# Optimization experiments

Measured on AMD Instinct MI355X. Metric: run time of the kernel, lower is better.

The kernel has to match this reference:

```python
import jax, jax.numpy as jnp
import numpy as np

L = 8       # num decoder layers
S = 192     # seq_len = h*w = 24*8
D = 512     # d_model
DFF = 2048  # dim_feedforward
H, W, BS = 24, 8, 16
EPS = 1e-5


def setup_inputs() -> dict:
    key = jax.random.key(0)
    ks = jax.random.split(key, 8)
    f = jax.random.normal
    return {
        "q_feat": f(ks[0], (BS, D * L, H, W), jnp.float32),
        "g_feat": f(ks[1], (BS, D * L, H, W), jnp.float32),
        "targets": jax.random.randint(ks[2], (BS,), 0, 8),
        "score_embed": f(ks[3], (L, S, S), jnp.float32) * 0.05,
        "fc0_w": f(ks[4], (L, D, D), jnp.float32) * (1.0 / np.sqrt(D)),
        "fc0_b": jnp.zeros((L, D), jnp.float32),
        "bn1_g": jnp.ones((L,), jnp.float32),
        "bn1_b": jnp.zeros((L,), jnp.float32),
        "fc2_w": f(ks[5], (L, DFF, S), jnp.float32) * (1.0 / np.sqrt(S)),
        "fc2_b": jnp.zeros((L, DFF), jnp.float32),
        "bn2_g": jnp.ones((L, DFF), jnp.float32),
        "bn2_b": jnp.zeros((L, DFF), jnp.float32),
        "fc3_w": f(ks[6], (L, DFF), jnp.float32) * (1.0 / np.sqrt(DFF)),
        "fc3_b": jnp.zeros((L,), jnp.float32),
        "bn3_g": jnp.ones((L,), jnp.float32),
        "bn3_b": jnp.zeros((L,), jnp.float32),
    }


def _layer(qf, gf, se, w0, b0, g1, b1, w2, b2, g2, bb2, w3, b3, g3, bb3):
    # qf: [q,s,d], gf: [k,s,d]; shared fc0 projection for query and key
    query = jnp.einsum('qsd,ed->qse', qf, w0) + b0
    key_ = jnp.einsum('ksd,ed->kse', gf, w0) + b0
    # 4D correlation volume masked by sigmoid of learned score embedding
    score = jnp.einsum('qtd,ksd->qkst', query, key_) * jax.nn.sigmoid(se)
    q, k = score.shape[0], score.shape[1]
    sc = score.reshape(q * k, S, S)
    cat = jnp.concatenate([sc.max(axis=1), sc.max(axis=2)], axis=-1)  # [qk, 2S]
    x = cat.reshape(-1, S)  # [2qk, S]  (matches torch view(-1,1,S))
    # bn1: single channel -> normalize over all elements (training-mode BN)
    x = g1 * (x - x.mean()) * jax.lax.rsqrt(x.var() + EPS) + b1
    x = x @ w2.T + b2  # [2qk, DFF]
    mu = x.mean(0)
    var = x.var(0)
    x = g2 * (x - mu) * jax.lax.rsqrt(var + EPS) + bb2
    x = jax.nn.relu(x)
    x = x @ w3 + b3  # [2qk]
    x = x.reshape(-1, 2).sum(-1)  # [qk]: sum of row-max branch and col-max branch
    x = g3 * (x - x.mean()) * jax.lax.rsqrt(x.var() + EPS) + bb3
    return x.reshape(q, k)


def reference(q_feat, g_feat, targets, score_embed, fc0_w, fc0_b, bn1_g, bn1_b,
              fc2_w, fc2_b, bn2_g, bn2_b, fc3_w, fc3_b, bn3_g, bn3_b):
    bs = q_feat.shape[0]
    qf = jnp.transpose(q_feat, (0, 2, 3, 1)).reshape(bs, S, D * L)
    gf = jnp.transpose(g_feat, (0, 2, 3, 1)).reshape(bs, S, D * L)
    score = None
    for i in range(L):  # fixed small layer loop; each layer has distinct params
        si = _layer(qf[..., i * D:(i + 1) * D], gf[..., i * D:(i + 1) * D],
                    score_embed[i], fc0_w[i], fc0_b[i], bn1_g[i], bn1_b[i],
                    fc2_w[i], fc2_b[i], bn2_g[i], bn2_b[i],
                    fc3_w[i], fc3_b[i], bn3_g[i], bn3_b[i])
        score = si if score is None else score + si
    pair_labels = (targets[:, None] == targets[None, :]).astype(jnp.float32)
    return score, pair_labels
```

## Files before the change

kernel.cpp:

```cpp
#include <hip/hip_runtime.h>
#include <hip/hip_bf16.h>


#define EPS_ 1e-5f

typedef __attribute__((ext_vector_type(8))) _Float16 fp16x8;
typedef __attribute__((ext_vector_type(4)))  float   f32x4;
typedef __attribute__((ext_vector_type(16))) float   f32x16;

__device__ __forceinline__ unsigned fkey(float f) {
    unsigned u = __float_as_uint(f);
    return (u & 0x80000000u) ? ~u : (u | 0x80000000u);
}
__device__ __forceinline__ float funkey(unsigned k) {
    return (k & 0x80000000u) ? __uint_as_float(k & 0x7FFFFFFFu)
                             : __uint_as_float(~k);
}
__device__ __forceinline__ void gld16(const void* gp, void* lp) {
    __builtin_amdgcn_global_load_lds(
        (const __attribute__((address_space(1))) unsigned*)gp,
        (__attribute__((address_space(3))) unsigned*)lp, 16, 0, 0);
}

__global__ __launch_bounds__(256) void k_sig(const float* __restrict__ se,
                                             float* __restrict__ sig) {
    int i = blockIdx.x * 256 + threadIdx.x;
    float4 v = *(const float4*)(se + (size_t)i * 4);
    float4 o;
    o.x = 1.f / (1.f + __expf(-v.x));
    o.y = 1.f / (1.f + __expf(-v.y));
    o.z = 1.f / (1.f + __expf(-v.z));
    o.w = 1.f / (1.f + __expf(-v.w));
    *(float4*)(sig + (size_t)i * 4) = o;
}

__global__ __launch_bounds__(256) void k_fc0(const float* __restrict__ qfeat,
                                             const float* __restrict__ gfeat,
                                             const float* __restrict__ w0,
                                             const float* __restrict__ b0,
                                             _Float16* __restrict__ Qh) {
    int bid = blockIdx.x;
    int et = bid & 1;  bid >>= 1;
    int tt = bid % 3;  bid /= 3;
    int b  = bid & 15; bid >>= 4;
    int l  = bid & 7;  bid >>= 3;
    int sel = bid;
    const float* feat  = sel ? gfeat : qfeat;
    const float* Af = feat + (size_t)b * 4096 * 192 + (size_t)l * 512 * 192;
    const float* Wf = w0 + (size_t)l * 262144;
    int t0 = tt * 64, e0 = et * 256;

    __shared__ __align__(16) char At[64 * 80];
    __shared__ __align__(16) char Bt[256 * 80];

    int tid = threadIdx.x;
    int lane = tid & 63;
    int w = tid >> 6;
    int half = lane >> 5;
    int lrow = lane & 31;

    f32x16 acc[2][2];
    #pragma unroll
    for (int mi = 0; mi < 2; mi++)
        #pragma unroll
        for (int ni = 0; ni < 2; ni++)
            #pragma unroll
            for (int r = 0; r < 16; r++) acc[mi][ni][r] = 0.f;

    for (int d0 = 0; d0 < 512; d0 += 32) {
        __syncthreads();
        {
            int tA = tid & 63;
            int dp = tid >> 6;
            #pragma unroll
            for (int r = 0; r < 4; r++) {
                int d = dp * 2 + r * 8;
                float v0 = Af[(size_t)(d0 + d) * 192 + t0 + tA];
                float v1 = Af[(size_t)(d0 + d + 1) * 192 + t0 + tA];
                _Float16 h2[2] = {(_Float16)v0, (_Float16)v1};
                *(unsigned*)(At + tA * 80 + d * 2) = *(unsigned*)h2;
            }
        }
        {
            #pragma unroll
            for (int p = 0; p < 8; p++) {
                int s = tid + p * 256;
                int e = s >> 3;
                int q = s & 7;
                float4 wv = *(const float4*)(Wf + (size_t)(e0 + e) * 512 + d0 + q * 4);
                _Float16 h[4] = {(_Float16)wv.x, (_Float16)wv.y, (_Float16)wv.z, (_Float16)wv.w};
                *(uint2*)(Bt + e * 80 + q * 8) = *(uint2*)h;
            }
        }
        __syncthreads();
        #pragma unroll
        for (int ks = 0; ks < 2; ks++) {
            int koff = ks * 32 + half * 16;
            fp16x8 a[2], bf[2];
            #pragma unroll
            for (int mi = 0; mi < 2; mi++)
                a[mi] = *(const fp16x8*)(At + (mi * 32 + lrow) * 80 + koff);
            #pragma unroll
            for (int ni = 0; ni < 2; ni++)
                bf[ni] = *(const fp16x8*)(Bt + (w * 64 + ni * 32 + lrow) * 80 + koff);
            #pragma unroll
            for (int mi = 0; mi < 2; mi++)
                #pragma unroll
                for (int ni = 0; ni < 2; ni++)
                    acc[mi][ni] = __builtin_amdgcn_mfma_f32_32x32x16_f16(a[mi], bf[ni], acc[mi][ni], 0, 0, 0);
        }
    }

    _Float16* Obase = Qh + ((size_t)(sel * 8 + l) * 16 + b) * 98304;
    #pragma unroll
    for (int ni = 0; ni < 2; ni++) {
        int e = e0 + w * 64 + ni * 32 + lrow;
        float bias = b0[l * 512 + e];
        #pragma unroll
        for (int mi = 0; mi < 2; mi++) {
            #pragma unroll
            for (int r = 0; r < 16; r++) {
                int t = t0 + mi * 32 + (r & 3) + 8 * (r >> 2) + 4 * half;
                Obase[(size_t)t * 512 + e] = (_Float16)(acc[mi][ni][r] + bias);
            }
        }
    }
}

__global__ __launch_bounds__(256) void k_cvt(const float* __restrict__ src,
                                             _Float16* __restrict__ dst) {
    int i = blockIdx.x * 256 + threadIdx.x;
    float4 v = *(const float4*)(src + (size_t)i * 4);
    _Float16 h[4] = {(_Float16)v.x, (_Float16)v.y, (_Float16)v.z, (_Float16)v.w};
    *(uint2*)(dst + (size_t)i * 4) = *(uint2*)h;
}

__global__ __launch_bounds__(256) void k_score(const _Float16* __restrict__ Qh,
                                               const float* __restrict__ sig,
                                               unsigned* __restrict__ xkey) {
    int bid = blockIdx.x;
    int l = bid / 576;
    int rem = bid - l * 576;
    int grp = rem / 96;
    int within = rem - grp * 96;
    int mt = within >> 2;
    int nt = grp * 4 + (within & 3);
    int m0 = mt * 128, n0 = nt * 128;

    const char* Ag = (const char*)(Qh + (size_t)(8 + l) * 1572864);
    const char* Bg = (const char*)(Qh + (size_t)l * 1572864);
    const float* sg = sig + (size_t)l * 36864;

    __shared__ __align__(16) char As[8192];
    __shared__ __align__(16) char Bs[8192];
    __shared__ unsigned tmaxL[4][64];
    __shared__ unsigned smaxL[4][64];

    int tid = threadIdx.x;
    int lane = tid & 63;
    int w = tid >> 6;
    int wm = w >> 1, wn = w & 1;

    f32x4 acc[4][4];
    #pragma unroll
    for (int mi = 0; mi < 4; mi++)
        #pragma unroll
        for (int nj = 0; nj < 4; nj++)
            #pragma unroll
            for (int r = 0; r < 4; r++) acc[mi][nj][r] = 0.f;

    int srow = lane >> 2;
    int sseg = ((lane & 3) ^ ((srow >> 1) & 3)) * 16;
    int c = lane & 15;
    int kqp = (((lane >> 4) ^ ((c >> 1) & 3))) * 16;

    for (int d0 = 0; d0 < 1024; d0 += 64) {
        __syncthreads();
        #pragma unroll
        for (int j = 0; j < 2; j++) {
            int r = w * 32 + j * 16 + srow;
            gld16(Ag + (size_t)(m0 + r) * 1024 + d0 + sseg, As + (w * 32 + j * 16) * 64);
            gld16(Bg + (size_t)(n0 + r) * 1024 + d0 + sseg, Bs + (w * 32 + j * 16) * 64);
        }
        __syncthreads();
        fp16x8 a[4], b[4];
        #pragma unroll
        for (int mi = 0; mi < 4; mi++)
            a[mi] = *(const fp16x8*)(As + (wm * 64 + mi * 16 + c) * 64 + kqp);
        #pragma unroll
        for (int nj = 0; nj < 4; nj++)
            b[nj] = *(const fp16x8*)(Bs + (wn * 64 + nj * 16 + c) * 64 + kqp);
        #pragma unroll
        for (int mi = 0; mi < 4; mi++)
            #pragma unroll
            for (int nj = 0; nj < 4; nj++)
                acc[mi][nj] = __builtin_amdgcn_mfma_f32_16x16x32_f16(a[mi], b[nj], acc[mi][nj], 0, 0, 0);
    }

    int gmb = m0 + wm * 64;
    int kk = gmb / 192, sb = gmb - kk * 192;
    int gnb = n0 + wn * 64;
    int qq = gnb / 192, tb = gnb - qq * 192;
    int rq = (lane >> 4) * 4;

    float rowm[4][4];
    float colm[4];
    #pragma unroll
    for (int mi = 0; mi < 4; mi++)
        #pragma unroll
        for (int r = 0; r < 4; r++) rowm[mi][r] = -3.4e38f;
    #pragma unroll
    for (int nj = 0; nj < 4; nj++) colm[nj] = -3.4e38f;

    #pragma unroll
    for (int mi = 0; mi < 4; mi++) {
        #pragma unroll
        for (int r = 0; r < 4; r++) {
            int s = sb + mi * 16 + rq + r;
            const float* srow_p = sg + (size_t)s * 192 + tb;
            #pragma unroll
            for (int nj = 0; nj < 4; nj++) {
                float m = srow_p[nj * 16 + c];
                float v = acc[mi][nj][r] * m;
                rowm[mi][r] = fmaxf(rowm[mi][r], v);
                colm[nj] = fmaxf(colm[nj], v);
            }
        }
    }
    #pragma unroll
    for (int nj = 0; nj < 4; nj++) {
        colm[nj] = fmaxf(colm[nj], __shfl_xor(colm[nj], 16));
        colm[nj] = fmaxf(colm[nj], __shfl_xor(colm[nj], 32));
    }
    if (lane < 16) {
        #pragma unroll
        for (int nj = 0; nj < 4; nj++)
            tmaxL[wm * 2 + wn][nj * 16 + lane] = fkey(colm[nj]);
    }
    #pragma unroll
    for (int st = 1; st <= 8; st <<= 1)
        #pragma unroll
        for (int mi = 0; mi < 4; mi++)
            #pragma unroll
            for (int r = 0; r < 4; r++)
                rowm[mi][r] = fmaxf(rowm[mi][r], __shfl_xor(rowm[mi][r], st));
    if (c == 0) {
        #pragma unroll
        for (int mi = 0; mi < 4; mi++)
            #pragma unroll
            for (int r = 0; r < 4; r++)
                smaxL[wm * 2 + wn][mi * 16 + rq + r] = fkey(rowm[mi][r]);
    }
    __syncthreads();

    #pragma unroll
    for (int rep = 0; rep < 2; rep++) {
        int idx = tid + rep * 256;
        int wp = idx >> 7;
        int which = (idx >> 6) & 1;
        int off = idx & 63;
        int wmf = wp >> 1, wnf = wp & 1;
        int kf = (m0 + wmf * 64) / 192, sbf = (m0 + wmf * 64) % 192;
        int qf = (n0 + wnf * 64) / 192, tbf = (n0 + wnf * 64) % 192;
        int jp = qf * 16 + kf;
        if (which == 0)
            atomicMax(&xkey[((size_t)l * 512 + 2 * jp) * 192 + tbf + off], tmaxL[wp][off]);
        else
            atomicMax(&xkey[((size_t)l * 512 + 2 * jp + 1) * 192 + sbf + off], smaxL[wp][off]);
    }
}

__global__ __launch_bounds__(256) void k_bn1s(const unsigned* __restrict__ xkey,
                                              float* __restrict__ bn1acc) {
    int l = blockIdx.x / 48;
    int b = blockIdx.x - l * 48;
    const unsigned* xk = xkey + (size_t)l * 98304 + b * 2048;
    int tid = threadIdx.x;
    uint4 v1 = *(const uint4*)(xk + tid * 8);
    uint4 v2 = *(const uint4*)(xk + tid * 8 + 4);
    float s = 0.f, s2 = 0.f;
    float e;
    e = funkey(v1.x); s += e; s2 += e * e;
    e = funkey(v1.y); s += e; s2 += e * e;
    e = funkey(v1.z); s += e; s2 += e * e;
    e = funkey(v1.w); s += e; s2 += e * e;
    e = funkey(v2.x); s += e; s2 += e * e;
    e = funkey(v2.y); s += e; s2 += e * e;
    e = funkey(v2.z); s += e; s2 += e * e;
    e = funkey(v2.w); s += e; s2 += e * e;
    #pragma unroll
    for (int o = 32; o; o >>= 1) { s += __shfl_down(s, o); s2 += __shfl_down(s2, o); }
    if ((tid & 63) == 0) {
        atomicAdd(&bn1acc[l * 2], s);
        atomicAdd(&bn1acc[l * 2 + 1], s2);
    }
}

__global__ __launch_bounds__(256) void k_bn1n(const unsigned* __restrict__ xkey,
                                              const float* __restrict__ bn1acc,
                                              const float* __restrict__ g1,
                                              const float* __restrict__ b1,
                                              _Float16* __restrict__ xh) {
    int idx = blockIdx.x * 256 + threadIdx.x;
    int l = idx / 24576;
    float mu = bn1acc[l * 2] * (1.f / 98304.f);
    float var = bn1acc[l * 2 + 1] * (1.f / 98304.f) - mu * mu;
    float a1 = g1[l] * rsqrtf(var + EPS_);
    float c1 = b1[l] - mu * a1;
    uint4 kv = *(const uint4*)(xkey + (size_t)idx * 4);
    _Float16 h[4];
    h[0] = (_Float16)(funkey(kv.x) * a1 + c1);
    h[1] = (_Float16)(funkey(kv.y) * a1 + c1);
    h[2] = (_Float16)(funkey(kv.z) * a1 + c1);
    h[3] = (_Float16)(funkey(kv.w) * a1 + c1);
    *(uint2*)(xh + (size_t)idx * 4) = *(uint2*)h;
}

__global__ __launch_bounds__(256) void k_fc2(const _Float16* __restrict__ xh,
                                             const _Float16* __restrict__ w2h,
                                             const float* __restrict__ b2,
                                             _Float16* __restrict__ hb,
                                             float* __restrict__ bn2sum,
                                             float* __restrict__ bn2sq) {
    int bid = blockIdx.x;
    int l = bid >> 6;
    int rem = bid & 63;
    int mt = rem & 3, nt = rem >> 2;
    int m0 = mt * 128, n0 = nt * 128;
    const char* Ag = (const char*)(xh + (size_t)l * 98304);
    const char* Bg = (const char*)(w2h + (size_t)l * 393216);

    __shared__ __align__(16) char As[8192];
    __shared__ __align__(16) char Bs[8192];

    int tid = threadIdx.x;
    int lane = tid & 63;
    int w = tid >> 6;
    int wm = w >> 1, wn = w & 1;

    f32x4 acc[4][4];
    #pragma unroll
    for (int mi = 0; mi < 4; mi++)
        #pragma unroll
        for (int nj = 0; nj < 4; nj++)
            #pragma unroll
            for (int r = 0; r < 4; r++) acc[mi][nj][r] = 0.f;

    int srow = lane >> 2;
    int sseg = ((lane & 3) ^ ((srow >> 1) & 3)) * 16;
    int c = lane & 15;
    int kqp = (((lane >> 4) ^ ((c >> 1) & 3))) * 16;

    for (int d0 = 0; d0 < 384; d0 += 64) {
        __syncthreads();
        #pragma unroll
        for (int j = 0; j < 2; j++) {
            int r = w * 32 + j * 16 + srow;
            gld16(Ag + (size_t)(m0 + r) * 384 + d0 + sseg, As + (w * 32 + j * 16) * 64);
            gld16(Bg + (size_t)(n0 + r) * 384 + d0 + sseg, Bs + (w * 32 + j * 16) * 64);
        }
        __syncthreads();
        fp16x8 a[4], b[4];
        #pragma unroll
        for (int mi = 0; mi < 4; mi++)
            a[mi] = *(const fp16x8*)(As + (wm * 64 + mi * 16 + c) * 64 + kqp);
        #pragma unroll
        for (int nj = 0; nj < 4; nj++)
            b[nj] = *(const fp16x8*)(Bs + (wn * 64 + nj * 16 + c) * 64 + kqp);
        #pragma unroll
        for (int mi = 0; mi < 4; mi++)
            #pragma unroll
            for (int nj = 0; nj < 4; nj++)
                acc[mi][nj] = __builtin_amdgcn_mfma_f32_16x16x32_f16(a[mi], b[nj], acc[mi][nj], 0, 0, 0);
    }

    int rq = (lane >> 4) * 4;
    _Float16* ho = hb + (size_t)l * 1048576;
    float colsum[4], colsq[4];
    #pragma unroll
    for (int nj = 0; nj < 4; nj++) { colsum[nj] = 0.f; colsq[nj] = 0.f; }
    #pragma unroll
    for (int nj = 0; nj < 4; nj++) {
        int gf = n0 + wn * 64 + nj * 16 + c;
        float bias = b2[l * 2048 + gf];
        #pragma unroll
        for (int mi = 0; mi < 4; mi++) {
            #pragma unroll
            for (int r = 0; r < 4; r++) {
                int gm = m0 + wm * 64 + mi * 16 + rq + r;
                float v = acc[mi][nj][r] + bias;
                ho[(size_t)gm * 2048 + gf] = (_Float16)v;
                colsum[nj] += v;
                colsq[nj] += v * v;
            }
        }
    }
    #pragma unroll
    for (int nj = 0; nj < 4; nj++) {
        colsum[nj] += __shfl_xor(colsum[nj], 16);
        colsum[nj] += __shfl_xor(colsum[nj], 32);
        colsq[nj]  += __shfl_xor(colsq[nj], 16);
        colsq[nj]  += __shfl_xor(colsq[nj], 32);
    }
    if (lane < 16) {
        #pragma unroll
        for (int nj = 0; nj < 4; nj++) {
            int gf = n0 + wn * 64 + nj * 16 + lane;
            atomicAdd(&bn2sum[l * 2048 + gf], colsum[nj]);
            atomicAdd(&bn2sq[l * 2048 + gf], colsq[nj]);
        }
    }
}

__global__ __launch_bounds__(256) void k_fc3(const _Float16* __restrict__ hb,
                                             const float* __restrict__ bn2sum,
                                             const float* __restrict__ bn2sq,
                                             const float* __restrict__ g2,
                                             const float* __restrict__ bb2,
                                             const float* __restrict__ w3,
                                             const float* __restrict__ b3,
                                             float* __restrict__ ybuf) {
    int n = blockIdx.x & 511;
    int l = blockIdx.x >> 9;
    const _Float16* h = hb + ((size_t)l * 512 + n) * 2048;
    int tid = threadIdx.x;
    int f0 = tid * 8;
    fp16x8 hv = *(const fp16x8*)(h + f0);
    float sum = 0.f;
    #pragma unroll
    for (int j = 0; j < 8; j++) {
        int f = f0 + j;
        float mu = bn2sum[l * 2048 + f] * (1.f / 512.f);
        float var = bn2sq[l * 2048 + f] * (1.f / 512.f) - mu * mu;
        float a2 = g2[l * 2048 + f] * rsqrtf(var + EPS_);
        float c2 = bb2[l * 2048 + f] - mu * a2;
        float v = (float)hv[j] * a2 + c2;
        v = fmaxf(v, 0.f);
        sum += v * w3[l * 2048 + f];
    }
    __shared__ float red[4];
    int lane = tid & 63, w = tid >> 6;
    #pragma unroll
    for (int o = 32; o; o >>= 1) sum += __shfl_down(sum, o);
    if (lane == 0) red[w] = sum;
    __syncthreads();
    if (tid == 0) ybuf[l * 512 + n] = red[0] + red[1] + red[2] + red[3] + b3[l];
}

__global__ __launch_bounds__(256) void k_final(const float* __restrict__ ybuf,
                                               const float* __restrict__ g3,
                                               const float* __restrict__ bb3,
                                               const int* __restrict__ targets,
                                               float* __restrict__ out) {
    int tid = threadIdx.x;
    __shared__ float red[8];
    float scoreacc = 0.f;
    for (int l = 0; l < 8; l++) {
        float z = ybuf[l * 512 + 2 * tid] + ybuf[l * 512 + 2 * tid + 1];
        float s = z, s2 = z * z;
        int lane = tid & 63, w = tid >> 6;
        #pragma unroll
        for (int o = 32; o; o >>= 1) { s += __shfl_down(s, o); s2 += __shfl_down(s2, o); }
        if (lane == 0) { red[w] = s; red[4 + w] = s2; }
        __syncthreads();
        float S1 = red[0] + red[1] + red[2] + red[3];
        float S2 = red[4] + red[5] + red[6] + red[7];
        float mu = S1 * (1.f / 256.f);
        float var = S2 * (1.f / 256.f) - mu * mu;
        float rstd = rsqrtf(var + EPS_);
        scoreacc += g3[l] * (z - mu) * rstd + bb3[l];
        __syncthreads();
    }
    out[tid] = scoreacc;
    int i = tid >> 4, j = tid & 15;
    out[256 + tid] = (targets[i] == targets[j]) ? 1.f : 0.f;
}

extern "C" void kernel_launch(void* const* d_in, const int* in_sizes, int n_in,
                              void* d_out, int out_size, void* d_ws, size_t ws_size,
                              hipStream_t stream) {
    const float* q_feat = (const float*)d_in[0];
    const float* g_feat = (const float*)d_in[1];
    const int*   targets = (const int*)d_in[2];
    const float* se     = (const float*)d_in[3];
    const float* fc0_w  = (const float*)d_in[4];
    const float* fc0_b  = (const float*)d_in[5];
    const float* bn1_g  = (const float*)d_in[6];
    const float* bn1_b  = (const float*)d_in[7];
    const float* fc2_w  = (const float*)d_in[8];
    const float* fc2_b  = (const float*)d_in[9];
    const float* bn2_g  = (const float*)d_in[10];
    const float* bn2_b  = (const float*)d_in[11];
    const float* fc3_w  = (const float*)d_in[12];
    const float* fc3_b  = (const float*)d_in[13];
    const float* bn3_g  = (const float*)d_in[14];
    const float* bn3_b  = (const float*)d_in[15];

    float* ws = (float*)d_ws;
    _Float16* Qh   = (_Float16*)ws;
    float*    sig  = ws + 12582912;
    unsigned* xkey = (unsigned*)(ws + 12877824);
    _Float16* xh   = (_Float16*)(ws + 13664256);
    _Float16* w2h  = (_Float16*)(ws + 14057472);
    _Float16* hb   = (_Float16*)(ws + 15630336);
    float* bn2sum = ws + 19824640;
    float* bn2sq  = ws + 19841024;
    float* bn1acc = ws + 19857408;
    float* ybuf   = ws + 19857424;
    float* out  = (float*)d_out;

    hipMemsetAsync(xkey, 0, 786432 * sizeof(unsigned), stream);
    hipMemsetAsync(bn2sum, 0, (2 * 16384 + 16) * sizeof(float), stream);
    k_sig<<<288, 256, 0, stream>>>(se, sig);
    k_cvt<<<3072, 256, 0, stream>>>(fc2_w, w2h);
    k_fc0<<<1536, 256, 0, stream>>>(q_feat, g_feat, fc0_w, fc0_b, Qh);
    k_score<<<4608, 256, 0, stream>>>(Qh, sig, xkey);
    k_bn1s<<<384, 256, 0, stream>>>(xkey, bn1acc);
    k_bn1n<<<768, 256, 0, stream>>>(xkey, bn1acc, bn1_g, bn1_b, xh);
    k_fc2<<<512, 256, 0, stream>>>(xh, w2h, fc2_b, hb, bn2sum, bn2sq);
    k_fc3<<<4096, 256, 0, stream>>>(hb, bn2sum, bn2sq, bn2_g, bn2_b, fc3_w, fc3_b, ybuf);
    k_final<<<1, 256, 0, stream>>>(ybuf, bn3_g, bn3_b, targets, out);
}
```

Before: 432.9 us.

## Rewrite score GEMM as 256x256 tiles with double-buffered LDS pipeline

Restructures the correlation-volume GEMM kernel from 128x128 tiles with 256 threads to 256x256 tiles with 512 threads. It uses 128KB of double-buffered LDS with async global-to-LDS loads interleaved between MFMA phases, and raises wave priority around the matrix math. The block order is also interleaved across layers. The larger tiles are meant to raise arithmetic intensity and hide load latency, at the cost of heavy register and LDS use, which limits occupancy.

```diff
diff --git a/kernel.cpp b/kernel.cpp
--- a/kernel.cpp
+++ b/kernel.cpp
@@ -135,138 +135,212 @@
     *(uint2*)(dst + (size_t)i * 4) = *(uint2*)h;
 }
 
-__global__ __launch_bounds__(256) void k_score(const _Float16* __restrict__ Qh,
-                                               const float* __restrict__ sig,
-                                               unsigned* __restrict__ xkey) {
+#define FENCE asm volatile("" ::: "memory")
+#define BAR() do { FENCE; __builtin_amdgcn_s_barrier(); FENCE; } while (0)
+
+__global__ __launch_bounds__(512, 2) void k_score(const _Float16* __restrict__ Qh,
+                                                  const float* __restrict__ sig,
+                                                  unsigned* __restrict__ xkey) {
     int bid = blockIdx.x;
-    int l = bid / 576;
-    int rem = bid - l * 576;
-    int grp = rem / 96;
-    int within = rem - grp * 96;
-    int mt = within >> 2;
-    int nt = grp * 4 + (within & 3);
-    int m0 = mt * 128, n0 = nt * 128;
+    int l = bid & 7;
+    int tau = bid >> 3;
+    int mt = tau % 12;
+    int nt = tau / 12;
+    int m0 = mt * 256, n0 = nt * 256;
 
     const char* Ag = (const char*)(Qh + (size_t)(8 + l) * 1572864);
     const char* Bg = (const char*)(Qh + (size_t)l * 1572864);
-    const float* sg = sig + (size_t)l * 36864;
-
-    __shared__ __align__(16) char As[8192];
-    __shared__ __align__(16) char Bs[8192];
-    __shared__ unsigned tmaxL[4][64];
-    __shared__ unsigned smaxL[4][64];
+
+    __shared__ __align__(16) char smem[131072];
 
     int tid = threadIdx.x;
     int lane = tid & 63;
     int w = tid >> 6;
-    int wm = w >> 1, wn = w & 1;
-
-    f32x4 acc[4][4];
-    #pragma unroll
-    for (int mi = 0; mi < 4; mi++)
+    int wm = w >> 2, wn = w & 3;
+    int c = lane & 15;
+    int hi4 = lane >> 4;
+
+    int pk0 = ((hi4)     ^ (c & 7)) * 16;
+    int pk1 = ((4 + hi4) ^ (c & 7)) * 16;
+    char* aBase = smem + wm * 16384 + c * 128;
+    char* bBase = smem + 65536 + (wn >> 1) * 16384 + ((wn & 1) * 64 + c) * 128;
+
+    int rl = lane >> 3;
+    int qsw = ((lane & 7) ^ rl) * 16;
+    const char* Asrc = Ag + (size_t)(m0 + w * 8 + rl) * 1024 + qsw;
+    const char* Bsrc = Bg + (size_t)(n0 + w * 8 + rl) * 1024 + qsw;
+    char* aSt = smem + w * 1024;
+    char* bSt = smem + 65536 + w * 1024;
+
+    f32x4 acc[8][4];
+    #pragma unroll
+    for (int mi = 0; mi < 8; mi++)
         #pragma unroll
         for (int nj = 0; nj < 4; nj++)
             #pragma unroll
             for (int r = 0; r < 4; r++) acc[mi][nj][r] = 0.f;
 
-    int srow = lane >> 2;
-    int sseg = ((lane & 3) ^ ((srow >> 1) & 3)) * 16;
-    int c = lane & 15;
-    int kqp = (((lane >> 4) ^ ((c >> 1) & 3))) * 16;
-
-    for (int d0 = 0; d0 < 1024; d0 += 64) {
-        __syncthreads();
-        #pragma unroll
-        for (int j = 0; j < 2; j++) {
-            int r = w * 32 + j * 16 + srow;
-            gld16(Ag + (size_t)(m0 + r) * 1024 + d0 + sseg, As + (w * 32 + j * 16) * 64);
-            gld16(Bg + (size_t)(n0 + r) * 1024 + d0 + sseg, Bs + (w * 32 + j * 16) * 64);
-        }
-        __syncthreads();
-        fp16x8 a[4], b[4];
-        #pragma unroll
-        for (int mi = 0; mi < 4; mi++)
-            a[mi] = *(const fp16x8*)(As + (wm * 64 + mi * 16 + c) * 64 + kqp);
-        #pragma unroll
-        for (int nj = 0; nj < 4; nj++)
-            b[nj] = *(const fp16x8*)(Bs + (wn * 64 + nj * 16 + c) * 64 + kqp);
-        #pragma unroll
-        for (int mi = 0; mi < 4; mi++)
-            #pragma unroll
-            for (int nj = 0; nj < 4; nj++)
-                acc[mi][nj] = __builtin_amdgcn_mfma_f32_16x16x32_f16(a[mi], b[nj], acc[mi][nj], 0, 0, 0);
-    }
-
-    int gmb = m0 + wm * 64;
-    int kk = gmb / 192, sb = gmb - kk * 192;
-    int gnb = n0 + wn * 64;
-    int qq = gnb / 192, tb = gnb - qq * 192;
-    int rq = (lane >> 4) * 4;
-
-    float rowm[4][4];
-    float colm[4];
-    #pragma unroll
-    for (int mi = 0; mi < 4; mi++)
+    fp16x8 a[4][2], b01[2][2], b23[2][2];
+
+    auto STA = [&](int t, int h) {
+        if (t < 8) {
+            const char* s = Asrc + (size_t)(h * 128) * 1024 + t * 128;
+            char* d = aSt + (t & 1) * 32768 + h * 16384;
+            gld16(s, d);
+            gld16(s + 64 * 1024, d + 8192);
+        }
+    };
+    auto STB = [&](int t, int h) {
+        if (t < 8) {
+            const char* s = Bsrc + (size_t)(h * 128) * 1024 + t * 128;
+            char* d = bSt + (t & 1) * 32768 + h * 16384;
+            gld16(s, d);
+            gld16(s + 64 * 1024, d + 8192);
+        }
+    };
+    auto LDA = [&](int t, int mh) {
+        const char* p = aBase + (t & 1) * 32768 + mh * 8192;
+        #pragma unroll
+        for (int m = 0; m < 4; m++) {
+            a[m][0] = *(const fp16x8*)(p + m * 2048 + pk0);
+            a[m][1] = *(const fp16x8*)(p + m * 2048 + pk1);
+        }
+    };
+    auto LDB = [&](int t, int nh, fp16x8 (&bb)[2][2]) {
+        const char* p = bBase + (t & 1) * 32768 + nh * 4096;
+        #pragma unroll
+        for (int n = 0; n < 2; n++) {
+            bb[n][0] = *(const fp16x8*)(p + n * 2048 + pk0);
+            bb[n][1] = *(const fp16x8*)(p + n * 2048 + pk1);
+        }
+    };
+    auto MM = [&](int mh, int nh, fp16x8 (&bb)[2][2]) {
+        #pragma unroll
+        for (int ks = 0; ks < 2; ks++)
+            #pragma unroll
+            for (int m = 0; m < 4; m++)
+                #pragma unroll
+                for (int n = 0; n < 2; n++)
+                    acc[mh * 4 + m][nh * 2 + n] = __builtin_amdgcn_mfma_f32_16x16x32_f16(
+                        a[m][ks], bb[n][ks], acc[mh * 4 + m][nh * 2 + n], 0, 0, 0);
+    };
+
+    STB(0, 0); STB(0, 1); STA(0, 0); STA(0, 1); STB(1, 0); STB(1, 1);
+    asm volatile("s_waitcnt vmcnt(4)" ::: "memory");
+    BAR();
+
+    #pragma unroll
+    for (int it = 0; it < 4; it++) {
+        int T = 2 * it, U = 2 * it + 1;
+        LDA(T, 0); LDB(T, 0, b01); STA(U, 0); BAR();
+        __builtin_amdgcn_s_setprio(1); MM(0, 0, b01); __builtin_amdgcn_s_setprio(0); BAR();
+        LDB(T, 1, b23); STA(U, 1); BAR();
+        __builtin_amdgcn_s_setprio(1); MM(0, 1, b23); __builtin_amdgcn_s_setprio(0); BAR();
+        LDA(T, 1); STB(T + 2, 0); BAR();
+        __builtin_amdgcn_s_setprio(1); MM(1, 0, b01); __builtin_amdgcn_s_setprio(0); BAR();
+        STB(T + 2, 1); BAR();
+        __builtin_amdgcn_s_setprio(1); MM(1, 1, b23); __builtin_amdgcn_s_setprio(0);
+        if (it < 3) { asm volatile("s_waitcnt vmcnt(4)" ::: "memory"); }
+        else        { asm volatile("s_waitcnt vmcnt(0)" ::: "memory"); }
+        BAR();
+        LDA(U, 0); LDB(U, 0, b01); STA(T + 2, 0); BAR();
+        __builtin_amdgcn_s_setprio(1); MM(0, 0, b01); __builtin_amdgcn_s_setprio(0); BAR();
+        LDB(U, 1, b23); STA(T + 2, 1); BAR();
+        __builtin_amdgcn_s_setprio(1); MM(0, 1, b23); __builtin_amdgcn_s_setprio(0); BAR();
+        LDA(U, 1); STB(T + 3, 0); BAR();
+        __builtin_amdgcn_s_setprio(1); MM(1, 0, b01); __builtin_amdgcn_s_setprio(0); BAR();
+        STB(T + 3, 1); BAR();
+        __builtin_amdgcn_s_setprio(1); MM(1, 1, b23); __builtin_amdgcn_s_setprio(0);
+        if (it < 3) { asm volatile("s_waitcnt vmcnt(4)" ::: "memory"); }
+        BAR();
+    }
+
+    int rq = hi4 * 4;
+    int gcb = n0 + wn * 64;
+    int qq = gcb / 192;
+    int tb = gcb - qq * 192;
+    (void)qq;
+    const float* sg = sig + (size_t)l * 36864;
+
+    float rowm[8][4];
+    float colm[2][4];
+    #pragma unroll
+    for (int mi = 0; mi < 8; mi++)
         #pragma unroll
         for (int r = 0; r < 4; r++) rowm[mi][r] = -3.4e38f;
     #pragma unroll
-    for (int nj = 0; nj < 4; nj++) colm[nj] = -3.4e38f;
-
-    #pragma unroll
-    for (int mi = 0; mi < 4; mi++) {
+    for (int h = 0; h < 2; h++)
+        #pragma unroll
+        for (int nj = 0; nj < 4; nj++) colm[h][nj] = -3.4e38f;
+
+    #pragma unroll
+    for (int mi = 0; mi < 8; mi++) {
+        int gm = m0 + wm * 128 + mi * 16;
+        int sb = gm % 192;
         #pragma unroll
         for (int r = 0; r < 4; r++) {
-            int s = sb + mi * 16 + rq + r;
-            const float* srow_p = sg + (size_t)s * 192 + tb;
+            const float* sp = sg + (size_t)(sb + rq + r) * 192 + tb;
             #pragma unroll
             for (int nj = 0; nj < 4; nj++) {
-                float m = srow_p[nj * 16 + c];
-                float v = acc[mi][nj][r] * m;
+                float v = acc[mi][nj][r] * sp[nj * 16 + c];
                 rowm[mi][r] = fmaxf(rowm[mi][r], v);
-                colm[nj] = fmaxf(colm[nj], v);
+                colm[mi >> 2][nj] = fmaxf(colm[mi >> 2][nj], v);
             }
         }
     }
     #pragma unroll
-    for (int nj = 0; nj < 4; nj++) {
-        colm[nj] = fmaxf(colm[nj], __shfl_xor(colm[nj], 16));
-        colm[nj] = fmaxf(colm[nj], __shfl_xor(colm[nj], 32));
-    }
-    if (lane < 16) {
-        #pragma unroll
-        for (int nj = 0; nj < 4; nj++)
-            tmaxL[wm * 2 + wn][nj * 16 + lane] = fkey(colm[nj]);
-    }
-    #pragma unroll
     for (int st = 1; st <= 8; st <<= 1)
         #pragma unroll
-        for (int mi = 0; mi < 4; mi++)
+        for (int mi = 0; mi < 8; mi++)
             #pragma unroll
             for (int r = 0; r < 4; r++)
                 rowm[mi][r] = fmaxf(rowm[mi][r], __shfl_xor(rowm[mi][r], st));
+    #pragma unroll
+    for (int h = 0; h < 2; h++)
+        #pragma unroll
+        for (int nj = 0; nj < 4; nj++) {
+            colm[h][nj] = fmaxf(colm[h][nj], __shfl_xor(colm[h][nj], 16));
+            colm[h][nj] = fmaxf(colm[h][nj], __shfl_xor(colm[h][nj], 32));
+        }
+
+    unsigned* red = (unsigned*)smem;
     if (c == 0) {
         #pragma unroll
-        for (int mi = 0; mi < 4; mi++)
+        for (int mi = 0; mi < 8; mi++)
             #pragma unroll
             for (int r = 0; r < 4; r++)
-                smaxL[wm * 2 + wn][mi * 16 + rq + r] = fkey(rowm[mi][r]);
+                red[w * 256 + mi * 16 + rq + r] = fkey(rowm[mi][r]);
+    }
+    if (lane < 16) {
+        #pragma unroll
+        for (int h = 0; h < 2; h++)
+            #pragma unroll
+            for (int nj = 0; nj < 4; nj++)
+                red[w * 256 + 128 + h * 64 + nj * 16 + lane] = fkey(colm[h][nj]);
     }
     __syncthreads();
-
-    #pragma unroll
-    for (int rep = 0; rep < 2; rep++) {
-        int idx = tid + rep * 256;
-        int wp = idx >> 7;
-        int which = (idx >> 6) & 1;
-        int off = idx & 63;
-        int wmf = wp >> 1, wnf = wp & 1;
-        int kf = (m0 + wmf * 64) / 192, sbf = (m0 + wmf * 64) % 192;
-        int qf = (n0 + wnf * 64) / 192, tbf = (n0 + wnf * 64) % 192;
-        int jp = qf * 16 + kf;
-        if (which == 0)
-            atomicMax(&xkey[((size_t)l * 512 + 2 * jp) * 192 + tbf + off], tmaxL[wp][off]);
-        else
-            atomicMax(&xkey[((size_t)l * 512 + 2 * jp + 1) * 192 + sbf + off], smaxL[wp][off]);
+    #pragma unroll
+    for (int pass = 0; pass < 4; pass++) {
+        int flat = pass * 512 + tid;
+        unsigned val = red[flat];
+        int ww = flat >> 8;
+        int rem = flat & 255;
+        int wmf = ww >> 2, wnf = ww & 3;
+        int gcbf = n0 + wnf * 64;
+        int qqf = gcbf / 192;
+        size_t addr;
+        if (rem < 128) {
+            int gmf = m0 + wmf * 128 + rem;
+            int kkf = gmf / 192;
+            int sf = gmf - kkf * 192;
+            addr = ((size_t)l * 512 + 2 * (qqf * 16 + kkf) + 1) * 192 + sf;
+        } else {
+            int ii = rem - 128;
+            int hh = ii >> 6, cc = ii & 63;
+            int kkf = (m0 + wmf * 128 + hh * 64) / 192;
+            addr = ((size_t)l * 512 + 2 * (qqf * 16 + kkf)) * 192 + (gcbf - qqf * 192) + cc;
+        }
+        atomicMax(&xkey[addr], val);
     }
 }
 
@@ -514,7 +588,7 @@
     k_sig<<<288, 256, 0, stream>>>(se, sig);
     k_cvt<<<3072, 256, 0, stream>>>(fc2_w, w2h);
     k_fc0<<<1536, 256, 0, stream>>>(q_feat, g_feat, fc0_w, fc0_b, Qh);
-    k_score<<<4608, 256, 0, stream>>>(Qh, sig, xkey);
+    k_score<<<1152, 512, 0, stream>>>(Qh, sig, xkey);
     k_bn1s<<<384, 256, 0, stream>>>(xkey, bn1acc);
     k_bn1n<<<768, 256, 0, stream>>>(xkey, bn1acc, bn1_g, bn1_b, xh);
     k_fc2<<<512, 256, 0, stream>>>(xh, w2h, fc2_b, hb, bn2sum, bn2sq);
```

Result: faster. 412.7 us (-4.7%).

## Pipeline score GEMM with triple-buffered LDS and fuse prep kernels

Applied to the files above, without the earlier changes.

Rewrites the correlation-score kernel as 512-thread blocks with 256x128 tiles and a three-slot LDS ring, so global-to-LDS loads for later K steps run while the current MFMAs execute. It uses explicit vmcnt waits, raw barriers and setprio. The sigmoid, weight conversion and two memsets are merged into one prep kernel to cut launch overhead. Block ordering changes so that layer index varies fastest. The large shared footprint may limit occupancy, and the hand-written waitcnt sequence is fragile.

```diff
diff --git a/kernel.cpp b/kernel.cpp
--- a/kernel.cpp
+++ b/kernel.cpp
@@ -22,16 +22,40 @@
         (__attribute__((address_space(3))) unsigned*)lp, 16, 0, 0);
 }
 
-__global__ __launch_bounds__(256) void k_sig(const float* __restrict__ se,
-                                             float* __restrict__ sig) {
-    int i = blockIdx.x * 256 + threadIdx.x;
-    float4 v = *(const float4*)(se + (size_t)i * 4);
-    float4 o;
-    o.x = 1.f / (1.f + __expf(-v.x));
-    o.y = 1.f / (1.f + __expf(-v.y));
-    o.z = 1.f / (1.f + __expf(-v.z));
-    o.w = 1.f / (1.f + __expf(-v.w));
-    *(float4*)(sig + (size_t)i * 4) = o;
+__global__ __launch_bounds__(256) void k_prep(const float* __restrict__ se,
+                                              float* __restrict__ sig,
+                                              const float* __restrict__ w2,
+                                              _Float16* __restrict__ w2h,
+                                              unsigned* __restrict__ xkey,
+                                              float* __restrict__ bn2z) {
+    int b = blockIdx.x;
+    int tid = threadIdx.x;
+    if (b < 3072) {
+        int i = b * 256 + tid;
+        float4 v = *(const float4*)(w2 + (size_t)i * 4);
+        _Float16 h[4] = {(_Float16)v.x, (_Float16)v.y, (_Float16)v.z, (_Float16)v.w};
+        *(uint2*)(w2h + (size_t)i * 4) = *(uint2*)h;
+    } else if (b < 3360) {
+        int i = (b - 3072) * 256 + tid;
+        float4 v = *(const float4*)(se + (size_t)i * 4);
+        float4 o;
+        o.x = 1.f / (1.f + __expf(-v.x));
+        o.y = 1.f / (1.f + __expf(-v.y));
+        o.z = 1.f / (1.f + __expf(-v.z));
+        o.w = 1.f / (1.f + __expf(-v.w));
+        *(float4*)(sig + (size_t)i * 4) = o;
+    } else if (b < 3552) {
+        int i = (b - 3360) * 256 + tid;
+        uint4 z = {0u, 0u, 0u, 0u};
+        uint4* p = (uint4*)xkey + (size_t)i * 4;
+        p[0] = z; p[1] = z; p[2] = z; p[3] = z;
+    } else {
+        int i = (b - 3552) * 256 + tid;
+        if (i < 8196) {
+            float4 z = {0.f, 0.f, 0.f, 0.f};
+            *(float4*)(bn2z + (size_t)i * 4) = z;
+        }
+    }
 }
 
 __global__ __launch_bounds__(256) void k_fc0(const float* __restrict__ qfeat,
@@ -127,39 +151,39 @@
     }
 }
 
-__global__ __launch_bounds__(256) void k_cvt(const float* __restrict__ src,
-                                             _Float16* __restrict__ dst) {
-    int i = blockIdx.x * 256 + threadIdx.x;
-    float4 v = *(const float4*)(src + (size_t)i * 4);
-    _Float16 h[4] = {(_Float16)v.x, (_Float16)v.y, (_Float16)v.z, (_Float16)v.w};
-    *(uint2*)(dst + (size_t)i * 4) = *(uint2*)h;
-}
-
-__global__ __launch_bounds__(256) void k_score(const _Float16* __restrict__ Qh,
-                                               const float* __restrict__ sig,
-                                               unsigned* __restrict__ xkey) {
+#define BARP() do { __builtin_amdgcn_s_barrier(); \
+                    __builtin_amdgcn_sched_barrier(0); } while (0)
+
+__global__ __launch_bounds__(512, 4) void k_score(const _Float16* __restrict__ Qh,
+                                                  const float* __restrict__ sig,
+                                                  unsigned* __restrict__ xkey) {
     int bid = blockIdx.x;
-    int l = bid / 576;
-    int rem = bid - l * 576;
-    int grp = rem / 96;
-    int within = rem - grp * 96;
-    int mt = within >> 2;
-    int nt = grp * 4 + (within & 3);
-    int m0 = mt * 128, n0 = nt * 128;
+    int l = bid & 7;
+    int tau = bid >> 3;
+    int mt = tau % 12;
+    int nt = tau / 12;
+    int m0 = mt * 256, n0 = nt * 128;
 
     const char* Ag = (const char*)(Qh + (size_t)(8 + l) * 1572864);
     const char* Bg = (const char*)(Qh + (size_t)l * 1572864);
-    const float* sg = sig + (size_t)l * 36864;
-
-    __shared__ __align__(16) char As[8192];
-    __shared__ __align__(16) char Bs[8192];
-    __shared__ unsigned tmaxL[4][64];
-    __shared__ unsigned smaxL[4][64];
+
+    __shared__ __align__(16) char smem[73728];
+    __shared__ unsigned tmaxL[8][64];
+    __shared__ unsigned smaxL[8][64];
 
     int tid = threadIdx.x;
     int lane = tid & 63;
     int w = tid >> 6;
     int wm = w >> 1, wn = w & 1;
+    int c = lane & 15;
+    int hi4 = lane >> 4;
+
+    int pk = (hi4 ^ (c & 3)) * 16;
+
+    int r4 = lane >> 2;
+    int qsw = ((lane & 3) ^ (r4 & 3)) * 16;
+    const char* AsrcL = Ag + (size_t)(m0 + w * 16 + r4) * 1024 + qsw;
+    const char* BsrcL = Bg + (size_t)(n0 + w * 16 + r4) * 1024 + qsw;
 
     f32x4 acc[4][4];
     #pragma unroll
@@ -169,39 +193,61 @@
             #pragma unroll
             for (int r = 0; r < 4; r++) acc[mi][nj][r] = 0.f;
 
-    int srow = lane >> 2;
-    int sseg = ((lane & 3) ^ ((srow >> 1) & 3)) * 16;
-    int c = lane & 15;
-    int kqp = (((lane >> 4) ^ ((c >> 1) & 3))) * 16;
-
-    for (int d0 = 0; d0 < 1024; d0 += 64) {
-        __syncthreads();
-        #pragma unroll
-        for (int j = 0; j < 2; j++) {
-            int r = w * 32 + j * 16 + srow;
-            gld16(Ag + (size_t)(m0 + r) * 1024 + d0 + sseg, As + (w * 32 + j * 16) * 64);
-            gld16(Bg + (size_t)(n0 + r) * 1024 + d0 + sseg, Bs + (w * 32 + j * 16) * 64);
-        }
-        __syncthreads();
-        fp16x8 a[4], b[4];
+    fp16x8 a[4], b[4];
+
+    auto STAGE = [&](int t) {
+        if (t < 16) {
+            int slot = t % 3;
+            const char* sa = AsrcL + t * 64;
+            char* da = smem + slot * 16384 + w * 1024;
+            gld16(sa, da);
+            gld16(sa + 131072, da + 8192);
+            gld16(BsrcL + t * 64, smem + 49152 + slot * 8192 + w * 1024);
+        }
+    };
+    auto LDAB = [&](int t) {
+        int slot = t % 3;
+        const char* pa = smem + slot * 16384 + (wm * 64 + c) * 64;
         #pragma unroll
         for (int mi = 0; mi < 4; mi++)
-            a[mi] = *(const fp16x8*)(As + (wm * 64 + mi * 16 + c) * 64 + kqp);
+            a[mi] = *(const fp16x8*)(pa + mi * 1024 + pk);
+        const char* pb = smem + 49152 + slot * 8192 + (wn * 64 + c) * 64;
         #pragma unroll
         for (int nj = 0; nj < 4; nj++)
-            b[nj] = *(const fp16x8*)(Bs + (wn * 64 + nj * 16 + c) * 64 + kqp);
+            b[nj] = *(const fp16x8*)(pb + nj * 1024 + pk);
+    };
+
+    STAGE(0); STAGE(1);
+    asm volatile("s_waitcnt vmcnt(3)");
+    BARP();
+
+    #pragma unroll
+    for (int t = 0; t < 16; t++) {
+        LDAB(t);
+        STAGE(t + 2);
+        BARP();
+        __builtin_amdgcn_s_setprio(1);
         #pragma unroll
         for (int mi = 0; mi < 4; mi++)
             #pragma unroll
             for (int nj = 0; nj < 4; nj++)
                 acc[mi][nj] = __builtin_amdgcn_mfma_f32_16x16x32_f16(a[mi], b[nj], acc[mi][nj], 0, 0, 0);
-    }
-
+        __builtin_amdgcn_s_setprio(0);
+        if (t < 14)       { asm volatile("s_waitcnt vmcnt(3)"); }
+        else if (t == 14) { asm volatile("s_waitcnt vmcnt(0)"); }
+        BARP();
+    }
+
+    __syncthreads();
+
+    int rq = hi4 * 4;
     int gmb = m0 + wm * 64;
     int kk = gmb / 192, sb = gmb - kk * 192;
+    (void)kk;
     int gnb = n0 + wn * 64;
     int qq = gnb / 192, tb = gnb - qq * 192;
-    int rq = (lane >> 4) * 4;
+    (void)qq;
+    const float* sg = sig + (size_t)l * 36864;
 
     float rowm[4][4];
     float colm[4];
@@ -217,11 +263,10 @@
         #pragma unroll
         for (int r = 0; r < 4; r++) {
             int s = sb + mi * 16 + rq + r;
-            const float* srow_p = sg + (size_t)s * 192 + tb;
+            const float* sp = sg + (size_t)s * 192 + tb;
             #pragma unroll
             for (int nj = 0; nj < 4; nj++) {
-                float m = srow_p[nj * 16 + c];
-                float v = acc[mi][nj][r] * m;
+                float v = acc[mi][nj][r] * sp[nj * 16 + c];
                 rowm[mi][r] = fmaxf(rowm[mi][r], v);
                 colm[nj] = fmaxf(colm[nj], v);
             }
@@ -235,7 +280,7 @@
     if (lane < 16) {
         #pragma unroll
         for (int nj = 0; nj < 4; nj++)
-            tmaxL[wm * 2 + wn][nj * 16 + lane] = fkey(colm[nj]);
+            tmaxL[w][nj * 16 + lane] = fkey(colm[nj]);
     }
     #pragma unroll
     for (int st = 1; st <= 8; st <<= 1)
@@ -249,24 +294,27 @@
         for (int mi = 0; mi < 4; mi++)
             #pragma unroll
             for (int r = 0; r < 4; r++)
-                smaxL[wm * 2 + wn][mi * 16 + rq + r] = fkey(rowm[mi][r]);
+                smaxL[w][mi * 16 + rq + r] = fkey(rowm[mi][r]);
     }
     __syncthreads();
 
     #pragma unroll
-    for (int rep = 0; rep < 2; rep++) {
-        int idx = tid + rep * 256;
-        int wp = idx >> 7;
+    for (int pass = 0; pass < 2; pass++) {
+        int idx = pass * 512 + tid;
+        int ww = idx >> 7;
         int which = (idx >> 6) & 1;
         int off = idx & 63;
-        int wmf = wp >> 1, wnf = wp & 1;
-        int kf = (m0 + wmf * 64) / 192, sbf = (m0 + wmf * 64) % 192;
-        int qf = (n0 + wnf * 64) / 192, tbf = (n0 + wnf * 64) % 192;
-        int jp = qf * 16 + kf;
-        if (which == 0)
-            atomicMax(&xkey[((size_t)l * 512 + 2 * jp) * 192 + tbf + off], tmaxL[wp][off]);
-        else
-            atomicMax(&xkey[((size_t)l * 512 + 2 * jp + 1) * 192 + sbf + off], smaxL[wp][off]);
+        int wmf = ww >> 1, wnf = ww & 1;
+        int gmf = m0 + wmf * 64;
+        int kkf = gmf / 192, sbf = gmf - kkf * 192;
+        int gnf = n0 + wnf * 64;
+        int qqf = gnf / 192, tbf = gnf - qqf * 192;
+        int jp = qqf * 16 + kkf;
+        size_t addr;
+        unsigned val;
+        if (which == 0) { val = tmaxL[ww][off]; addr = ((size_t)l * 512 + 2 * jp) * 192 + tbf + off; }
+        else            { val = smaxL[ww][off]; addr = ((size_t)l * 512 + 2 * jp + 1) * 192 + sbf + off; }
+        atomicMax(&xkey[addr], val);
     }
 }
 
@@ -509,12 +557,9 @@
     float* ybuf   = ws + 19857424;
     float* out  = (float*)d_out;
 
-    hipMemsetAsync(xkey, 0, 786432 * sizeof(unsigned), stream);
-    hipMemsetAsync(bn2sum, 0, (2 * 16384 + 16) * sizeof(float), stream);
-    k_sig<<<288, 256, 0, stream>>>(se, sig);
-    k_cvt<<<3072, 256, 0, stream>>>(fc2_w, w2h);
+    k_prep<<<3585, 256, 0, stream>>>(se, sig, fc2_w, w2h, xkey, bn2sum);
     k_fc0<<<1536, 256, 0, stream>>>(q_feat, g_feat, fc0_w, fc0_b, Qh);
-    k_score<<<4608, 256, 0, stream>>>(Qh, sig, xkey);
+    k_score<<<2304, 512, 0, stream>>>(Qh, sig, xkey);
     k_bn1s<<<384, 256, 0, stream>>>(xkey, bn1acc);
     k_bn1n<<<768, 256, 0, stream>>>(xkey, bn1acc, bn1_g, bn1_b, xh);
     k_fc2<<<512, 256, 0, stream>>>(xh, w2h, fc2_b, hb, bn2sum, bn2sq);
```

Result: faster. 409.6 us (-5.4%).
